# Kernel optimization log

Measured on AMD Instinct MI355X. Metric: run time of the kernel, lower is better.

## Reference

```python
import jax, jax.numpy as jnp
import numpy as np

DIM = 1024
HEADS = 16
DIM_HEAD = 64
SCALE = DIM_HEAD ** -0.5
RMS_SCALE = DIM ** 0.5


def rms_norm(x, gamma):
    # F.normalize(x, dim=-1) * sqrt(dim) * gamma
    norm = jnp.sqrt(jnp.sum(x * x, axis=-1, keepdims=True))
    normed = x / jnp.maximum(norm, 1e-12)
    return normed * RMS_SCALE * gamma


def setup_inputs() -> dict:
    key = jax.random.key(0)
    ks = jax.random.split(key, 7)
    b, n, m = 2, 2048, 2048
    x = jax.random.normal(ks[0], (b, n, DIM), dtype=jnp.float32)
    context = jax.random.normal(ks[1], (b, m, DIM), dtype=jnp.float32)
    normalized_scores_kv = jax.random.uniform(ks[2], (b, m), dtype=jnp.float32)
    mask = jnp.ones((b, m), dtype=bool)
    gamma = jnp.ones((DIM,), dtype=jnp.float32)
    s = 0.02
    Wq = jax.random.normal(ks[3], (DIM, HEADS * DIM_HEAD), dtype=jnp.float32) * s
    Wkv = jax.random.normal(ks[4], (DIM, 2 * HEADS * DIM_HEAD), dtype=jnp.float32) * s
    Wout = jax.random.normal(ks[5], (HEADS * DIM_HEAD, DIM), dtype=jnp.float32) * s
    return {"x": x, "context": context, "normalized_scores_kv": normalized_scores_kv,
            "mask": mask, "gamma": gamma, "Wq": Wq, "Wkv": Wkv, "Wout": Wout}


def reference(x, context, normalized_scores_kv, mask, gamma, Wq, Wkv, Wout):
    b, n, _ = x.shape
    m = context.shape[1]
    xn = rms_norm(x, gamma)
    cn = rms_norm(context, gamma)
    q = xn @ Wq                     # [b, n, h*d]
    kv = cn @ Wkv                   # [b, m, 2*h*d]
    k, v = jnp.split(kv, 2, axis=-1)
    def to_heads(t):
        return t.reshape(t.shape[0], t.shape[1], HEADS, DIM_HEAD).transpose(0, 2, 1, 3)
    q, k, v = to_heads(q), to_heads(k), to_heads(v)   # [b, h, n, d]
    v = v * normalized_scores_kv[:, None, :, None]
    q = q * SCALE
    sim = jnp.einsum('bhid,bhjd->bhij', q, k)
    neg = -jnp.finfo(sim.dtype).max
    sim = jnp.where(mask[:, None, None, :], sim, neg)
    attn = jax.nn.softmax(sim, axis=-1)
    out = jnp.einsum('bhij,bhjd->bhid', attn, v)
    out = out.transpose(0, 2, 1, 3).reshape(b, n, HEADS * DIM_HEAD)
    return out @ Wout
```

## Files before the change

kernel.cpp:

```cpp
#include <hip/hip_runtime.h>
#include <hip/hip_bf16.h>

typedef _Float16 f16;
typedef _Float16 f16x2 __attribute__((ext_vector_type(2)));
typedef _Float16 f16x4 __attribute__((ext_vector_type(4)));
typedef _Float16 f16x8 __attribute__((ext_vector_type(8)));
typedef __fp16 h16x2 __attribute__((ext_vector_type(2)));
typedef float f32x4 __attribute__((ext_vector_type(4)));

#define DIM 1024
#define SEQ 2048
#define NB 2
#define NH 16
#define DHEAD 64
#define KVB 64
#define QBLK 128
#define NT (SEQ / KVB)

__device__ __forceinline__ void gl_lds16(const f16* g, f16* l) {
  __builtin_amdgcn_global_load_lds(
      (const __attribute__((address_space(1))) unsigned int*)(g),
      (__attribute__((address_space(3))) unsigned int*)(l), 16, 0, 0);
}

__device__ __forceinline__ f16x2 pkrtz(float a, float b) {
  h16x2 t = __builtin_amdgcn_cvt_pkrtz(a, b);
  return __builtin_bit_cast(f16x2, t);
}

__global__ __launch_bounds__(256) void rms_cast_kernel(
    const float* __restrict__ x, const float* __restrict__ ctx,
    const float* __restrict__ gamma, f16* __restrict__ xn, f16* __restrict__ cn)
{
  int row = blockIdx.x;
  const float* src; f16* dst;
  if (row < NB * SEQ) { src = x + (size_t)row * DIM;              dst = xn + (size_t)row * DIM; }
  else                { src = ctx + (size_t)(row - NB*SEQ) * DIM; dst = cn + (size_t)(row - NB*SEQ) * DIM; }
  int t = threadIdx.x;
  float4 v = ((const float4*)src)[t];
  float ss = v.x*v.x + v.y*v.y + v.z*v.z + v.w*v.w;
  #pragma unroll
  for (int m = 1; m < 64; m <<= 1) ss += __shfl_xor(ss, m, 64);
  __shared__ float red[4];
  if ((t & 63) == 0) red[t >> 6] = ss;
  __syncthreads();
  float total = red[0] + red[1] + red[2] + red[3];
  float scale = 32.0f / fmaxf(sqrtf(total), 1e-12f);
  float4 gv = ((const float4*)gamma)[t];
  dst[4*t+0] = (f16)(v.x * scale * gv.x);
  dst[4*t+1] = (f16)(v.y * scale * gv.y);
  dst[4*t+2] = (f16)(v.z * scale * gv.z);
  dst[4*t+3] = (f16)(v.w * scale * gv.w);
}

__global__ __launch_bounds__(256) void transpose_cast3_kernel(
    const float* __restrict__ Wq, const float* __restrict__ Wkv, const float* __restrict__ Wout,
    f16* __restrict__ WqT, f16* __restrict__ WkvT, f16* __restrict__ WoT)
{
  __shared__ float tile[32][33];
  int bx = blockIdx.x;
  const float* W; f16* Wt; int N, n0;
  if (bx < 32)      { W = Wq;   Wt = WqT;  N = 1024; n0 = bx * 32; }
  else if (bx < 96) { W = Wkv;  Wt = WkvT; N = 2048; n0 = (bx - 32) * 32; }
  else              { W = Wout; Wt = WoT;  N = 1024; n0 = (bx - 96) * 32; }
  int k0 = blockIdx.y * 32;
  int tx = threadIdx.x & 31, ty = threadIdx.x >> 5;
  #pragma unroll
  for (int i = 0; i < 32; i += 8)
    tile[ty + i][tx] = W[(size_t)(k0 + ty + i) * N + n0 + tx];
  __syncthreads();
  #pragma unroll
  for (int i = 0; i < 32; i += 8)
    Wt[(size_t)(n0 + ty + i) * 1024 + k0 + tx] = (f16)tile[tx][ty + i];
}

template<int MODE>
__global__ __launch_bounds__(256, 4) void gemm_kernel(
    const f16* __restrict__ A, const f16* __restrict__ Bt,
    const float* __restrict__ scores,
    f16* __restrict__ o16a, f16* __restrict__ o16b, float* __restrict__ o32)
{
  __shared__ f16 As[64][32];
  __shared__ f16 Bs[128][32];
  const int m0 = blockIdx.x * 64, n0 = blockIdx.y * 128;
  const int tid = threadIdx.x, lane = tid & 63, w = tid >> 6;
  const int wm = w >> 1, wn = w & 1;
  const int g = lane >> 4, c = lane & 15;

  const int sr4 = lane >> 2, sp = lane & 3;
  const int ra  = w*16 + sr4;
  const int rb0 = w*32 + sr4, rb1 = w*32 + 16 + sr4;
  const f16* gA  = A  + (size_t)(m0 + ra)  * 1024 + (sp ^ (ra  & 3)) * 8;
  const f16* gB0 = Bt + (size_t)(n0 + rb0) * 1024 + (sp ^ (rb0 & 3)) * 8;
  const f16* gB1 = Bt + (size_t)(n0 + rb1) * 1024 + (sp ^ (rb1 & 3)) * 8;
  f16* dA  = &As[w*16][0];
  f16* dB0 = &Bs[w*32][0];
  f16* dB1 = &Bs[w*32 + 16][0];

  f32x4 acc[2][4] = {};

  for (int k0 = 0; k0 < 1024; k0 += 32) {
    __syncthreads();
    gl_lds16(gA  + k0, dA);
    gl_lds16(gB0 + k0, dB0);
    gl_lds16(gB1 + k0, dB1);
    __syncthreads();
    f16x8 af[2], bf[4];
    #pragma unroll
    for (int tm = 0; tm < 2; tm++) af[tm] = *(const f16x8*)&As[wm*32 + tm*16 + c][(g ^ (c & 3)) * 8];
    #pragma unroll
    for (int tn = 0; tn < 4; tn++) bf[tn] = *(const f16x8*)&Bs[wn*64 + tn*16 + c][(g ^ (c & 3)) * 8];
    #pragma unroll
    for (int tm = 0; tm < 2; tm++)
      #pragma unroll
      for (int tn = 0; tn < 4; tn++)
        acc[tm][tn] = __builtin_amdgcn_mfma_f32_16x16x32_f16(af[tm], bf[tn], acc[tm][tn], 0, 0, 0);
  }

  #pragma unroll
  for (int tm = 0; tm < 2; tm++) {
    #pragma unroll
    for (int tn = 0; tn < 4; tn++) {
      int rg0 = m0 + wm*32 + tm*16 + g*4;
      int cg  = n0 + wn*64 + tn*16 + c;
      int b = rg0 >> 11, s0 = rg0 & 2047;
      if (MODE == 0) {
        int h = cg >> 6, d = cg & 63;
        #pragma unroll
        for (int r = 0; r < 4; r++)
          o16a[(((size_t)(b*NH + h))*SEQ + s0 + r)*DHEAD + d] =
              (f16)(acc[tm][tn][r] * 0.18033688011112043f);
      } else if (MODE == 1) {
        int hh = (cg & 1023) >> 6, d = cg & 63;
        if (cg < 1024) {
          #pragma unroll
          for (int r = 0; r < 4; r++)
            o16a[(((size_t)(b*NH + hh))*SEQ + s0 + r)*DHEAD + d] = (f16)acc[tm][tn][r];
        } else {
          float4 sc = *(const float4*)(scores + b*SEQ + s0);
          f16x4 pk;
          pk[0] = (f16)(acc[tm][tn][0] * sc.x);
          pk[1] = (f16)(acc[tm][tn][1] * sc.y);
          pk[2] = (f16)(acc[tm][tn][2] * sc.z);
          pk[3] = (f16)(acc[tm][tn][3] * sc.w);
          *(f16x4*)(o16b + (((size_t)(b*NH + hh))*DHEAD + d)*SEQ + s0) = pk;
        }
      } else {
        #pragma unroll
        for (int r = 0; r < 4; r++)
          o32[(size_t)(rg0 + r) * 1024 + cg] = acc[tm][tn][r];
      }
    }
  }
}

#define PT_OFF 32768

__global__ __launch_bounds__(256, 3) void attn_kernel(
    const f16* __restrict__ Q, const f16* __restrict__ K,
    const f16* __restrict__ Vt, f16* __restrict__ O)
{
  __shared__ __align__(16) char L[51200];

  const int bid = blockIdx.x;
  const int xcd = bid & 7, i = bid >> 3;
  const int bh  = xcd*4 + (i >> 4);
  const int q0  = (i & 15) * QBLK;
  const int tid = threadIdx.x, lane = tid & 63, w = tid >> 6;
  const int g = lane >> 4, c = lane & 15;

  const f16* Qb  = Q  + (size_t)bh * SEQ * DHEAD;
  const f16* Kb  = K  + (size_t)bh * SEQ * DHEAD;
  const f16* Vbt = Vt + (size_t)bh * DHEAD * SEQ;

  f16x8 aq[2][2];
  #pragma unroll
  for (int qs = 0; qs < 2; qs++) {
    int qr = q0 + w*32 + qs*16 + c;
    aq[qs][0] = *(const f16x8*)(Qb + (size_t)qr * DHEAD + g*8);
    aq[qs][1] = *(const f16x8*)(Qb + (size_t)qr * DHEAD + 32 + g*8);
  }

  f32x4 oacc[2][4] = {};
  float mr[2] = {-1e30f, -1e30f};
  float lr[2] = {0.f, 0.f};

  const int sj = lane >> 3;
  const int sl = (lane & 7) ^ sj;
  const f16* kgb0 = Kb  + (size_t)(w*16     + sj) * DHEAD + sl*8;
  const f16* kgb1 = Kb  + (size_t)(w*16 + 8 + sj) * DHEAD + sl*8;
  const f16* vgb0 = Vbt + (size_t)(w*16     + sj) * SEQ   + sl*8;
  const f16* vgb1 = Vbt + (size_t)(w*16 + 8 + sj) * SEQ   + sl*8;

  const unsigned ptb = PT_OFF + w*4608;
  const unsigned sw0 = ((g     ^ (c & 7)) << 4);
  const unsigned sw1 = (((4+g) ^ (c & 7)) << 4);

  f32x4 s[4][2];
  f16x4 pk[2][4];

#define STAGE(kv0v, slot) {                                                        \
    gl_lds16(kgb0 + (size_t)(kv0v)*DHEAD, (f16*)(L + (slot) + w*2048));            \
    gl_lds16(kgb1 + (size_t)(kv0v)*DHEAD, (f16*)(L + (slot) + w*2048 + 1024));     \
    gl_lds16(vgb0 + (kv0v),               (f16*)(L + (slot) + 8192 + w*2048));     \
    gl_lds16(vgb1 + (kv0v),               (f16*)(L + (slot) + 8192 + w*2048 + 1024)); }

#define QK_TILE(slot) {                                                            \
    _Pragma("unroll")                                                              \
    for (int ct = 0; ct < 4; ct++) {                                               \
      f16x8 k0 = *(const f16x8*)(L + (slot) + (ct*16 + c)*128 + sw0);              \
      f16x8 k1 = *(const f16x8*)(L + (slot) + (ct*16 + c)*128 + sw1);              \
      f32x4 z = {0.f, 0.f, 0.f, 0.f};                                              \
      s[ct][0] = __builtin_amdgcn_mfma_f32_16x16x32_f16(k0, aq[0][0], z, 0, 0, 0); \
      s[ct][0] = __builtin_amdgcn_mfma_f32_16x16x32_f16(k1, aq[0][1], s[ct][0], 0, 0, 0); \
      s[ct][1] = __builtin_amdgcn_mfma_f32_16x16x32_f16(k0, aq[1][0], z, 0, 0, 0); \
      s[ct][1] = __builtin_amdgcn_mfma_f32_16x16x32_f16(k1, aq[1][1], s[ct][1], 0, 0, 0); \
    } }

#define SOFTMAX() {                                                                \
    float mx0 = -1e30f, mx1 = -1e30f;                                              \
    _Pragma("unroll")                                                              \
    for (int ct = 0; ct < 4; ct++) {                                               \
      mx0 = fmaxf(mx0, fmaxf(fmaxf(s[ct][0][0], s[ct][0][1]), fmaxf(s[ct][0][2], s[ct][0][3]))); \
      mx1 = fmaxf(mx1, fmaxf(fmaxf(s[ct][1][0], s[ct][1][1]), fmaxf(s[ct][1][2], s[ct][1][3]))); \
    }                                                                              \
    mx0 = fmaxf(mx0, __shfl_xor(mx0, 16, 64)); mx0 = fmaxf(mx0, __shfl_xor(mx0, 32, 64)); \
    mx1 = fmaxf(mx1, __shfl_xor(mx1, 16, 64)); mx1 = fmaxf(mx1, __shfl_xor(mx1, 32, 64)); \
    if (!__all((mx0 <= mr[0] + 8.f) && (mx1 <= mr[1] + 8.f))) {                    \
      _Pragma("unroll")                                                            \
      for (int qs = 0; qs < 2; qs++) {                                             \
        float mxq = qs ? mx1 : mx0;                                                \
        float mn = fmaxf(mr[qs], mxq);                                             \
        float al = __builtin_amdgcn_exp2f(mr[qs] - mn);                            \
        mr[qs] = mn; lr[qs] *= al;                                                 \
        _Pragma("unroll")                                                          \
        for (int dt = 0; dt < 4; dt++)                                             \
          { oacc[qs][dt][0]*=al; oacc[qs][dt][1]*=al; oacc[qs][dt][2]*=al; oacc[qs][dt][3]*=al; } \
      }                                                                            \
    }                                                                              \
    _Pragma("unroll")                                                              \
    for (int qs = 0; qs < 2; qs++) {                                               \
      float rs = 0.f;                                                              \
      _Pragma("unroll")                                                            \
      for (int ct = 0; ct < 4; ct++) {                                             \
        float p0 = __builtin_amdgcn_exp2f(s[ct][qs][0] - mr[qs]);                  \
        float p1 = __builtin_amdgcn_exp2f(s[ct][qs][1] - mr[qs]);                  \
        float p2 = __builtin_amdgcn_exp2f(s[ct][qs][2] - mr[qs]);                  \
        float p3 = __builtin_amdgcn_exp2f(s[ct][qs][3] - mr[qs]);                  \
        rs += (p0 + p1) + (p2 + p3);                                               \
        f16x2 lo = pkrtz(p0, p1), hi = pkrtz(p2, p3);                              \
        pk[qs][ct] = __builtin_shufflevector(lo, hi, 0, 1, 2, 3);                  \
      }                                                                            \
      rs += __shfl_xor(rs, 16, 64); rs += __shfl_xor(rs, 32, 64);                  \
      lr[qs] += rs;                                                                \
    } }

#define PWRITE() {                                                                 \
    _Pragma("unroll")                                                              \
    for (int qs = 0; qs < 2; qs++)                                                 \
      _Pragma("unroll")                                                            \
      for (int ct = 0; ct < 4; ct++)                                               \
        *(f16x4*)(L + ptb + (qs*16 + c)*144 + ct*32 + g*8) = pk[qs][ct]; }

#define PV_TILE(slot) {                                                            \
    _Pragma("unroll")                                                              \
    for (int kc = 0; kc < 2; kc++) {                                               \
      f16x8 bp0 = *(const f16x8*)(L + ptb + c*144        + kc*64 + g*16);          \
      f16x8 bp1 = *(const f16x8*)(L + ptb + (16 + c)*144 + kc*64 + g*16);          \
      unsigned swc = kc ? sw1 : sw0;                                               \
      _Pragma("unroll")                                                            \
      for (int dt = 0; dt < 4; dt++) {                                             \
        f16x8 vf = *(const f16x8*)(L + (slot) + 8192 + (dt*16 + c)*128 + swc);     \
        oacc[0][dt] = __builtin_amdgcn_mfma_f32_16x16x32_f16(vf, bp0, oacc[0][dt], 0, 0, 0); \
        oacc[1][dt] = __builtin_amdgcn_mfma_f32_16x16x32_f16(vf, bp1, oacc[1][dt], 0, 0, 0); \
      }                                                                            \
    } }

  STAGE(0, 0);
  __syncthreads();

  for (int t = 0; t < NT; ++t) {
    const unsigned cur = (t & 1) ? 16384u : 0u;
    const unsigned nxt = cur ^ 16384u;
    if (t + 1 < NT) STAGE((t + 1) * KVB, nxt);
    __builtin_amdgcn_s_setprio(1);
    QK_TILE(cur);
    __builtin_amdgcn_s_setprio(0);
    SOFTMAX();
    PWRITE();
    __builtin_amdgcn_s_setprio(1);
    PV_TILE(cur);
    __builtin_amdgcn_s_setprio(0);
    __syncthreads();
  }

  #pragma unroll
  for (int qs = 0; qs < 2; qs++) {
    float inv = 1.0f / lr[qs];
    #pragma unroll
    for (int dt = 0; dt < 4; dt++) {
      f16x4 ov;
      ov[0] = (f16)(oacc[qs][dt][0] * inv);
      ov[1] = (f16)(oacc[qs][dt][1] * inv);
      ov[2] = (f16)(oacc[qs][dt][2] * inv);
      ov[3] = (f16)(oacc[qs][dt][3] * inv);
      *(f16x4*)(L + ptb + (qs*16 + c)*144 + (dt*16 + 4*g)*2) = ov;
    }
  }
  {
    const int b = bh >> 4, h = bh & 15;
    #pragma unroll
    for (int p = 0; p < 2; p++) {
      int ql = p*16 + (lane >> 2), chq = lane & 3;
      const char* src = L + ptb + ql*144 + chq*32;
      float4 a0 = *(const float4*)src;
      float4 a1 = *(const float4*)(src + 16);
      f16* dst = O + ((size_t)(b*SEQ + q0 + w*32 + ql))*1024 + h*64 + chq*16;
      *(float4*)dst = a0;
      *(float4*)(dst + 8) = a1;
    }
  }
#undef STAGE
#undef QK_TILE
#undef SOFTMAX
#undef PWRITE
#undef PV_TILE
}

extern "C" void kernel_launch(void* const* d_in, const int* in_sizes, int n_in,
                              void* d_out, int out_size, void* d_ws, size_t ws_size,
                              hipStream_t stream)
{
  const float* x      = (const float*)d_in[0];
  const float* ctx    = (const float*)d_in[1];
  const float* scores = (const float*)d_in[2];
  const float* gamma  = (const float*)d_in[4];
  const float* Wq     = (const float*)d_in[5];
  const float* Wkv    = (const float*)d_in[6];
  const float* Wout   = (const float*)d_in[7];
  float* out = (float*)d_out;

  char* ws = (char*)d_ws;
  const size_t MB = 1024 * 1024;
  f16* xn   = (f16*)(ws);
  f16* cn   = (f16*)(ws + 8*MB);
  f16* WqT  = (f16*)(ws + 16*MB);
  f16* WkvT = (f16*)(ws + 18*MB);
  f16* WoT  = (f16*)(ws + 22*MB);
  f16* qb   = (f16*)(ws + 24*MB);
  f16* kb   = (f16*)(ws + 32*MB);
  f16* vbT  = (f16*)(ws + 40*MB);
  f16* ao   = xn;

  rms_cast_kernel<<<NB*SEQ*2, 256, 0, stream>>>(x, ctx, gamma, xn, cn);
  transpose_cast3_kernel<<<dim3(128, 32), 256, 0, stream>>>(Wq, Wkv, Wout, WqT, WkvT, WoT);
  gemm_kernel<0><<<dim3(64, 8),  256, 0, stream>>>(xn, WqT,  nullptr, qb, nullptr, nullptr);
  gemm_kernel<1><<<dim3(64, 16), 256, 0, stream>>>(cn, WkvT, scores,  kb, vbT,     nullptr);
  attn_kernel<<<dim3(512), 256, 0, stream>>>(qb, kb, vbT, ao);
  gemm_kernel<2><<<dim3(64, 8),  256, 0, stream>>>(ao, WoT,  nullptr, nullptr, nullptr, out);
}
```

Baseline: 142.4 us.

## Enlarge GEMM tiles to 128x128 with double-buffered K=64 LDS staging

The projection GEMM kernel moves from 64x128 tiles with a K-step of 32 to 128x128 tiles with a K-step of 64. It double-buffers the direct global-to-LDS loads in a 64KB shared buffer, so each next stage is fetched while the current one is computed, and drops one barrier per iteration. Each wave now holds a 4x4 MFMA accumulator block with an XOR-swizzled LDS layout. The aim is more operand reuse and overlap of loads with compute, at the cost of higher register and LDS use, lower occupancy (launch bounds 2) and half as many blocks.

Measured after the change: 129.5 us. -9.0%, faster.

```diff
diff --git a/kernel.cpp b/kernel.cpp
--- a/kernel.cpp
+++ b/kernel.cpp
@@ -75,53 +75,66 @@
 }
 
 template<int MODE>
-__global__ __launch_bounds__(256, 4) void gemm_kernel(
+__global__ __launch_bounds__(256, 2) void gemm_kernel(
     const f16* __restrict__ A, const f16* __restrict__ Bt,
     const float* __restrict__ scores,
     f16* __restrict__ o16a, f16* __restrict__ o16b, float* __restrict__ o32)
 {
-  __shared__ f16 As[64][32];
-  __shared__ f16 Bs[128][32];
-  const int m0 = blockIdx.x * 64, n0 = blockIdx.y * 128;
+  __shared__ __align__(16) char L[65536];
+
+  const int m0 = blockIdx.x * 128, n0 = blockIdx.y * 128;
   const int tid = threadIdx.x, lane = tid & 63, w = tid >> 6;
   const int wm = w >> 1, wn = w & 1;
   const int g = lane >> 4, c = lane & 15;
 
-  const int sr4 = lane >> 2, sp = lane & 3;
-  const int ra  = w*16 + sr4;
-  const int rb0 = w*32 + sr4, rb1 = w*32 + 16 + sr4;
-  const f16* gA  = A  + (size_t)(m0 + ra)  * 1024 + (sp ^ (ra  & 3)) * 8;
-  const f16* gB0 = Bt + (size_t)(n0 + rb0) * 1024 + (sp ^ (rb0 & 3)) * 8;
-  const f16* gB1 = Bt + (size_t)(n0 + rb1) * 1024 + (sp ^ (rb1 & 3)) * 8;
-  f16* dA  = &As[w*16][0];
-  f16* dB0 = &Bs[w*32][0];
-  f16* dB1 = &Bs[w*32 + 16][0];
-
-  f32x4 acc[2][4] = {};
-
-  for (int k0 = 0; k0 < 1024; k0 += 32) {
-    __syncthreads();
-    gl_lds16(gA  + k0, dA);
-    gl_lds16(gB0 + k0, dB0);
-    gl_lds16(gB1 + k0, dB1);
-    __syncthreads();
-    f16x8 af[2], bf[4];
+  const int sj = lane >> 3;
+  const int sl = (lane & 7) ^ sj;
+  const f16* gA = A  + (size_t)(m0 + w*32 + sj) * 1024 + sl * 8;
+  const f16* gB = Bt + (size_t)(n0 + w*32 + sj) * 1024 + sl * 8;
+  const unsigned stA = w * 4096;
+  const unsigned stB = 16384 + w * 4096;
+
+  const unsigned swz = (c & 7) << 4;
+
+  f32x4 acc[4][4] = {};
+
+#define GSTAGE(k0v, buf) {                                                      \
+    _Pragma("unroll")                                                           \
+    for (int i2 = 0; i2 < 4; i2++) {                                            \
+      gl_lds16(gA + (size_t)(8*i2) * 1024 + (k0v), (f16*)(L + (buf) + stA + i2*1024)); \
+      gl_lds16(gB + (size_t)(8*i2) * 1024 + (k0v), (f16*)(L + (buf) + stB + i2*1024)); \
+    } }
+
+  GSTAGE(0, 0)
+  __syncthreads();
+
+  for (int t = 0; t < 16; ++t) {
+    const unsigned cur = (t & 1) ? 32768u : 0u;
+    if (t + 1 < 16) GSTAGE((t + 1) * 64, cur ^ 32768u)
     #pragma unroll
-    for (int tm = 0; tm < 2; tm++) af[tm] = *(const f16x8*)&As[wm*32 + tm*16 + c][(g ^ (c & 3)) * 8];
-    #pragma unroll
-    for (int tn = 0; tn < 4; tn++) bf[tn] = *(const f16x8*)&Bs[wn*64 + tn*16 + c][(g ^ (c & 3)) * 8];
-    #pragma unroll
-    for (int tm = 0; tm < 2; tm++)
+    for (int kk = 0; kk < 2; kk++) {
+      f16x8 af[4], bf[4];
+      #pragma unroll
+      for (int tm = 0; tm < 4; tm++)
+        af[tm] = *(const f16x8*)(L + cur + (wm*64 + tm*16 + c)*128 + (((kk*4 + g) << 4) ^ swz));
       #pragma unroll
       for (int tn = 0; tn < 4; tn++)
-        acc[tm][tn] = __builtin_amdgcn_mfma_f32_16x16x32_f16(af[tm], bf[tn], acc[tm][tn], 0, 0, 0);
-  }
-
-  #pragma unroll
-  for (int tm = 0; tm < 2; tm++) {
+        bf[tn] = *(const f16x8*)(L + cur + 16384 + (wn*64 + tn*16 + c)*128 + (((kk*4 + g) << 4) ^ swz));
+      #pragma unroll
+      for (int tm = 0; tm < 4; tm++)
+        #pragma unroll
+        for (int tn = 0; tn < 4; tn++)
+          acc[tm][tn] = __builtin_amdgcn_mfma_f32_16x16x32_f16(af[tm], bf[tn], acc[tm][tn], 0, 0, 0);
+    }
+    __syncthreads();
+  }
+#undef GSTAGE
+
+  #pragma unroll
+  for (int tm = 0; tm < 4; tm++) {
     #pragma unroll
     for (int tn = 0; tn < 4; tn++) {
-      int rg0 = m0 + wm*32 + tm*16 + g*4;
+      int rg0 = m0 + wm*64 + tm*16 + g*4;
       int cg  = n0 + wn*64 + tn*16 + c;
       int b = rg0 >> 11, s0 = rg0 & 2047;
       if (MODE == 0) {
@@ -354,8 +367,8 @@
 
   rms_cast_kernel<<<NB*SEQ*2, 256, 0, stream>>>(x, ctx, gamma, xn, cn);
   transpose_cast3_kernel<<<dim3(128, 32), 256, 0, stream>>>(Wq, Wkv, Wout, WqT, WkvT, WoT);
-  gemm_kernel<0><<<dim3(64, 8),  256, 0, stream>>>(xn, WqT,  nullptr, qb, nullptr, nullptr);
-  gemm_kernel<1><<<dim3(64, 16), 256, 0, stream>>>(cn, WkvT, scores,  kb, vbT,     nullptr);
+  gemm_kernel<0><<<dim3(32, 8),  256, 0, stream>>>(xn, WqT,  nullptr, qb, nullptr, nullptr);
+  gemm_kernel<1><<<dim3(32, 16), 256, 0, stream>>>(cn, WkvT, scores,  kb, vbT,     nullptr);
   attn_kernel<<<dim3(512), 256, 0, stream>>>(qb, kb, vbT, ao);
-  gemm_kernel<2><<<dim3(64, 8),  256, 0, stream>>>(ao, WoT,  nullptr, nullptr, nullptr, out);
-}
+  gemm_kernel<2><<<dim3(32, 8),  256, 0, stream>>>(ao, WoT,  nullptr, nullptr, nullptr, out);
+}
```
